# Performance work log

Measured on AMD Instinct MI355X. Metric: run time of the kernel, lower is better.

## Reference

```python
import math
import jax, jax.numpy as jnp
import numpy as np

LAMBDA_TV = 0.005
LAMBDA_WAV = 0.005
MAX_ITER = 15
LEVELS = 3
TV_ITERS = 5  # prox_tv called with num_iter=5 in forward
S2 = math.sqrt(2.0)


def _fft2c(x):
    # x: (B, 2, H, W) real/imag channels -> centered 2D FFT, same layout
    xc = x[:, 0] + 1j * x[:, 1]
    kc = jnp.fft.fftshift(
        jnp.fft.fft2(jnp.fft.ifftshift(xc, axes=(-2, -1)), norm='ortho'),
        axes=(-2, -1))
    return jnp.stack([kc.real, kc.imag], axis=1)


def _ifft2c(x):
    xc = x[:, 0] + 1j * x[:, 1]
    ic = jnp.fft.fftshift(
        jnp.fft.ifft2(jnp.fft.ifftshift(xc, axes=(-2, -1)), norm='ortho'),
        axes=(-2, -1))
    return jnp.stack([ic.real, ic.imag], axis=1)


def _grad(x):
    # x: (N, 1, H, W) -> forward differences, (N, 2, H, W); last row/col zero
    dx = jnp.pad(x[:, :, :, 1:] - x[:, :, :, :-1], ((0, 0), (0, 0), (0, 0), (0, 1)))
    dy = jnp.pad(x[:, :, 1:, :] - x[:, :, :-1, :], ((0, 0), (0, 0), (0, 1), (0, 0)))
    return jnp.concatenate([dx, dy], axis=1)


def _div(p):
    # adjoint of _grad with the exact boundary handling of the torch code
    px, py = p[:, 0:1], p[:, 1:2]
    div_x = jnp.concatenate(
        [px[:, :, :, 0:1], px[:, :, :, 1:-1] - px[:, :, :, :-2], -px[:, :, :, -2:-1]],
        axis=-1)
    div_y = jnp.concatenate(
        [py[:, :, 0:1, :], py[:, :, 1:-1, :] - py[:, :, :-2, :], -py[:, :, -2:-1, :]],
        axis=2)
    return div_x + div_y


def _prox_tv(x, lam):
    # Chambolle dual iteration, applied per channel (vectorized over B*C)
    B, C, H, W = x.shape
    xc = x.reshape(B * C, 1, H, W)
    tau = 0.25

    def body(p, _):
        g = _grad(xc - lam * _div(p))
        pn = p + tau * g
        nrm = jnp.sqrt(jnp.sum(pn * pn, axis=1, keepdims=True) + 1e-8)
        return pn / jnp.maximum(nrm, 1.0), None

    p0 = jnp.zeros((B * C, 2, H, W), x.dtype)
    p, _ = jax.lax.scan(body, p0, None, length=TV_ITERS)
    return (xc - lam * _div(p)).reshape(B, C, H, W)


def _dwt2(x):
    x_lo = (x[:, :, :, ::2] + x[:, :, :, 1::2]) / S2
    x_hi = (x[:, :, :, ::2] - x[:, :, :, 1::2]) / S2
    ll = (x_lo[:, :, ::2] + x_lo[:, :, 1::2]) / S2
    lh = (x_lo[:, :, ::2] - x_lo[:, :, 1::2]) / S2
    hl = (x_hi[:, :, ::2] + x_hi[:, :, 1::2]) / S2
    hh = (x_hi[:, :, ::2] - x_hi[:, :, 1::2]) / S2
    return ll, (lh, hl, hh)


def _interleave(even, odd, axis):
    s = jnp.stack([even, odd], axis=axis + 1)
    shp = list(even.shape)
    shp[axis] *= 2
    return s.reshape(shp)


def _idwt2(ll, lh, hl, hh):
    x_lo = _interleave((ll + lh) / S2, (ll - lh) / S2, axis=2)  # rows
    x_hi = _interleave((hl + hh) / S2, (hl - hh) / S2, axis=2)
    return _interleave((x_lo + x_hi) / S2, (x_lo - x_hi) / S2, axis=3)  # cols


def _soft(x, t):
    return jnp.sign(x) * jnp.maximum(jnp.abs(x) - t, 0.0)


def setup_inputs() -> dict:
    key = jax.random.key(0)
    k1, k2 = jax.random.split(key)
    B, H, W = 16, 320, 320
    y = jax.random.normal(k1, (B, 2, H, W), jnp.float32)
    mask = (jax.random.uniform(k2, (B, 1, H, W)) < 0.3).astype(jnp.float32)
    return {"y": y, "mask": mask}


def reference(y, mask):
    def step(carry, _):
        x, z, t = carry
        # projected gradient for data fidelity (step_size = 1.0)
        g = _ifft2c(mask * (mask * _fft2c(z) - y))
        z_step = z - g
        # TV prox
        x_tv = _prox_tv(z_step, LAMBDA_TV)
        # wavelet decomposition + soft-threshold of detail subbands
        cur = x_tv
        details = []
        for _lvl in range(LEVELS):
            cur, d = _dwt2(cur)
            details.append(tuple(_soft(c, LAMBDA_WAV) for c in d))
        x_new = cur
        for d in reversed(details):
            x_new = _idwt2(x_new, *d)
        # FISTA momentum
        t_new = (1.0 + jnp.sqrt(1.0 + 4.0 * t * t)) / 2.0
        z_new = x_new + (t - 1.0) / t_new * (x_new - x)
        return (x_new, z_new, t_new), None

    x0 = _ifft2c(y)
    (x, _, _), _ = jax.lax.scan(jax.checkpoint(step), (x0, x0, jnp.float32(1.0)),
                                None, length=MAX_ITER)
    return x
```

## Files before the change

kernel.cpp:

```cpp
#include <hip/hip_runtime.h>
#include <math.h>

constexpr int WID  = 320;
constexpr int HWc  = 320 * 320;
constexpr int NIMG = 16;
constexpr int NSL  = 32;
constexpr int NTOT = NIMG * 2 * HWc;
constexpr float LAM_TV  = 0.005f;
constexpr float LAM_WAV = 0.005f;

__device__ __forceinline__ float softt(float v) {
    float a = fmaxf(fabsf(v) - LAM_WAV, 0.f);
    return copysignf(a, v);
}

__device__ __forceinline__ float fast_rsq(float x) {
    float r;
    asm volatile("v_rsq_f32 %0, %1" : "=v"(r) : "v"(x));
    return r;
}

struct Tw { float tc, ts; float stc[6], sts[6]; };

__global__ void build_tw(float* tb) {
    const int lane = threadIdx.x;
#pragma unroll
    for (int g = 0; g < 2; g++) {
        const float sgn = g ? 1.f : -1.f;
        float* p = tb + g * 14 * 64;
        float ts, tc;
        __sincosf(sgn * 6.283185307179586f * (float)lane / 320.f, &ts, &tc);
        p[lane] = tc; p[64 + lane] = ts;
#pragma unroll
        for (int s = 0; s < 6; s++) {
            int h = 32 >> s;
            int j = lane & (h - 1);
            float ang = sgn * 3.14159265358979323f * (float)j / (float)h;
            float ss, cc;
            __sincosf(ang, &ss, &cc);
            p[(2 + s) * 64 + lane] = cc;
            p[(8 + s) * 64 + lane] = ss;
        }
    }
}

__device__ __forceinline__ Tw load_tw(const float* __restrict__ tb, int lane) {
    Tw tw;
    tw.tc = tb[lane];
    tw.ts = tb[64 + lane];
#pragma unroll
    for (int s = 0; s < 6; s++) {
        tw.stc[s] = tb[(2 + s) * 64 + lane];
        tw.sts[s] = tb[(8 + s) * 64 + lane];
    }
    return tw;
}

template<int SGN>
__device__ __forceinline__ void fft320_core(const float (&vr)[5], const float (&vi)[5],
                                            float (&Cr)[5], float (&Ci)[5],
                                            const Tw& tw, int lane) {
    const float cw1 = 0.30901699437494745f, sw1 = 0.9510565162951535f;
    const float cw2 = -0.8090169943749475f, sw2 = 0.5877852522924731f;
    const float cwt[5] = {1.f, cw1, cw2, cw2, cw1};
    const float swt[5] = {0.f, sw1, sw2, -sw2, -sw1};
    Cr[0] = vr[0] + vr[1] + vr[2] + vr[3] + vr[4];
    Ci[0] = vi[0] + vi[1] + vi[2] + vi[3] + vi[4];
#pragma unroll
    for (int k = 1; k < 5; k++) {
        float ar = vr[0], ai = vi[0];
#pragma unroll
        for (int m = 1; m < 5; m++) {
            int j = (m * k) % 5;
            float wr_ = cwt[j], wi_ = (float)SGN * swt[j];
            ar += vr[m] * wr_ - vi[m] * wi_;
            ai += vr[m] * wi_ + vi[m] * wr_;
        }
        Cr[k] = ar; Ci[k] = ai;
    }
    float twr = 1.f, twi = 0.f;
#pragma unroll
    for (int k = 1; k < 5; k++) {
        float nr = twr * tw.tc - twi * tw.ts;
        twi = twr * tw.ts + twi * tw.tc;
        twr = nr;
        float r = Cr[k] * twr - Ci[k] * twi;
        Ci[k]   = Cr[k] * twi + Ci[k] * twr;
        Cr[k]   = r;
    }
#pragma unroll
    for (int s = 0; s < 6; s++) {
        int h = 32 >> s;
        bool up = (lane & h) != 0;
#pragma unroll
        for (int k = 0; k < 5; k++) {
            float orr = __shfl_xor(Cr[k], h);
            float oii = __shfl_xor(Ci[k], h);
            if (up) {
                float dr = orr - Cr[k], di = oii - Ci[k];
                Cr[k] = dr * tw.stc[s] - di * tw.sts[s];
                Ci[k] = dr * tw.sts[s] + di * tw.stc[s];
            } else {
                Cr[k] += orr;
                Ci[k] += oii;
            }
        }
    }
}

template<int SGN, int EPI>
__global__ __launch_bounds__(256) void fft_row(const float* __restrict__ in,
                                               float* __restrict__ out,
                                               const float* __restrict__ aux1,
                                               float* __restrict__ out2,
                                               const float* __restrict__ twb) {
    const int lane = threadIdx.x & 63;
    const int wv   = threadIdx.x >> 6;
    const int L    = blockIdx.x * 4 + wv;
    const int img  = L / 320;
    const int l    = L - img * 320;
    const size_t ibase = (size_t)img * 2 * HWc;
    const float* pre = in + ibase + (size_t)l * WID;
    const float* pim = pre + HWc;
    const int k1 = (int)(__brev((unsigned)lane) >> 26);

    Tw tw = load_tw(twb, lane);

    float vr[5], vi[5];
    const float sgn_in = (lane & 1) ? -1.f : 1.f;
#pragma unroll
    for (int m = 0; m < 5; m++) {
        int n = lane + 64 * m;
        vr[m] = sgn_in * pre[n];
        vi[m] = sgn_in * pim[n];
    }
    float zr[5], zi[5];
    if (EPI == 2) {
#pragma unroll
        for (int k = 0; k < 5; k++) {
            int idxs = 5 * k1 + k + l * WID;
            zr[k] = aux1[ibase + idxs];
            zi[k] = aux1[ibase + HWc + idxs];
        }
    }

    float Cr[5], Ci[5];
    fft320_core<SGN>(vr, vi, Cr, Ci, tw, lane);

    float* qre = out + ibase + (size_t)l * WID;
    float* qim = qre + HWc;
    const float scale = 0.05590169943749474f;
#pragma unroll
    for (int k = 0; k < 5; k++) {
        int kout = 5 * k1 + k;
        float s2 = (kout & 1) ? -scale : scale;
        float re = s2 * Cr[k];
        float im = s2 * Ci[k];
        const int idxs = kout + l * WID;
        if (EPI == 2) {
            re = zr[k] - re;
            im = zi[k] - im;
        }
        qre[kout] = re;
        qim[kout] = im;
        if (EPI == 3) {
            out2[ibase + idxs]       = re;
            out2[ibase + HWc + idxs] = im;
        }
    }
}

constexpr int CB   = 8;
constexpr int CPAD = CB + 1;

template<int SGN>
__device__ __forceinline__ void fft_line_lds(float (*tile)[320][CPAD], int cl,
                                             int lane, const Tw& tw) {
    float vr[5], vi[5], Cr[5], Ci[5];
    const float sgn_in = (lane & 1) ? -1.f : 1.f;
#pragma unroll
    for (int m = 0; m < 5; m++) {
        int n = lane + 64 * m;
        vr[m] = sgn_in * tile[0][n][cl];
        vi[m] = sgn_in * tile[1][n][cl];
    }
    fft320_core<SGN>(vr, vi, Cr, Ci, tw, lane);
    const int k1 = (int)(__brev((unsigned)lane) >> 26);
    const float scale = 0.05590169943749474f;
#pragma unroll
    for (int k = 0; k < 5; k++) {
        int kout = 5 * k1 + k;
        float s2 = (kout & 1) ? -scale : scale;
        tile[0][kout][cl] = s2 * Cr[k];
        tile[1][kout][cl] = s2 * Ci[k];
    }
}

template<int MODE>
__global__ __launch_bounds__(512) void fft_col(const float* __restrict__ in,
                                               float* __restrict__ out,
                                               const float* __restrict__ y,
                                               const float* __restrict__ mask,
                                               const float* __restrict__ twb) {
    __shared__ float tile[2][320][CPAD];
    const int tid = threadIdx.x;
    const int bpi = WID / CB;
    const int img = blockIdx.x / bpi;
    const int c0  = (blockIdx.x - img * bpi) * CB;
    const size_t ibase = (size_t)img * 2 * HWc;
    constexpr int C4 = CB / 4;
    constexpr int NE = 320 * C4;

#pragma unroll
    for (int comp = 0; comp < 2; comp++) {
        const float* p = in + ibase + (size_t)comp * HWc + c0;
        for (int i = tid; i < NE; i += 512) {
            int row = i >> 1, cg = (i & 1) << 2;
            float4 v = *(const float4*)(p + row * WID + cg);
            float* t = &tile[comp][row][cg];
            t[0] = v.x; t[1] = v.y; t[2] = v.z; t[3] = v.w;
        }
    }
    __syncthreads();

    const int lane = tid & 63;
    const int wv   = tid >> 6;

    if (MODE == 1) {
        Tw twf = load_tw(twb, lane);
        fft_line_lds<-1>(tile, wv, lane, twf);
        __syncthreads();
        const float* pm  = mask + (size_t)img * HWc + c0;
        const float* pyr = y + ibase + c0;
        const float* pyi = y + ibase + HWc + c0;
        for (int i = tid; i < NE; i += 512) {
            int row = i >> 1, cg = (i & 1) << 2;
            float4 m4 = *(const float4*)(pm  + row * WID + cg);
            float4 yr = *(const float4*)(pyr + row * WID + cg);
            float4 yi = *(const float4*)(pyi + row * WID + cg);
            float* tr = &tile[0][row][cg];
            float* ti = &tile[1][row][cg];
            tr[0] = m4.x * (m4.x * tr[0] - yr.x);
            tr[1] = m4.y * (m4.y * tr[1] - yr.y);
            tr[2] = m4.z * (m4.z * tr[2] - yr.z);
            tr[3] = m4.w * (m4.w * tr[3] - yr.w);
            ti[0] = m4.x * (m4.x * ti[0] - yi.x);
            ti[1] = m4.y * (m4.y * ti[1] - yi.y);
            ti[2] = m4.z * (m4.z * ti[2] - yi.z);
            ti[3] = m4.w * (m4.w * ti[3] - yi.w);
        }
        __syncthreads();
    }
    {
        Tw twi = load_tw(twb + 14 * 64, lane);
        fft_line_lds<1>(tile, wv, lane, twi);
    }
    __syncthreads();
#pragma unroll
    for (int comp = 0; comp < 2; comp++) {
        float* p = out + ibase + (size_t)comp * HWc + c0;
        for (int i = tid; i < NE; i += 512) {
            int row = i >> 1, cg = (i & 1) << 2;
            const float* t = &tile[comp][row][cg];
            *(float4*)(p + row * WID + cg) = make_float4(t[0], t[1], t[2], t[3]);
        }
    }
}

constexpr int HALO = 4;
constexpr int TIR = 8;
constexpr int TVR = TIR + 2 * HALO;
constexpr int TIC = 48;
constexpr int TCOLS = 7;
constexpr int TROWS = WID / TIR;
constexpr int TPS = TROWS * TCOLS;

template<bool EDGE>
__device__ __forceinline__ void tv_core(const float* __restrict__ g, int gi0, int gj,
                                        float (&uf)[TIR]) {
    float z_[TVR], px_[TVR], py_[TVR];
    const bool colin = !EDGE || ((unsigned)gj < (unsigned)WID);
#pragma unroll
    for (int r = 0; r < TVR; r++) {
        int gi = gi0 + r;
        float v = 0.f;
        if (!EDGE) {
            v = g[gi * WID + gj];
        } else {
            bool in = colin && ((unsigned)gi < (unsigned)WID);
            if (in) v = g[gi * WID + gj];
        }
        z_[r] = v; px_[r] = 0.f; py_[r] = 0.f;
    }
    const bool gj_le0 = EDGE && (gj <= 0);
    const bool gj_hi  = EDGE && (gj >= WID - 1);
    const bool gx_on  = !EDGE || (gj < WID - 1);

#pragma clang loop unroll(disable)
    for (int it = 0; it < 5; it++) {
        float ucur, unext;
        {
            float pxm = __shfl_up(px_[0], 1);
            float divx, divy;
            if (!EDGE) {
                divx = px_[0] - pxm;
                divy = 0.f;
            } else {
                int gi = gi0;
                divx = gj_le0 ? px_[0] : (gj_hi ? -pxm : px_[0] - pxm);
                divy = (gi <= 0) ? py_[0] : ((gi >= WID - 1) ? -py_[0] : 0.f);
            }
            ucur = z_[0] - LAM_TV * (divx + divy);
        }
#pragma unroll
        for (int r = 0; r < TVR - 1; r++) {
            {
                float pxm = __shfl_up(px_[r + 1], 1);
                float divx, divy;
                if (!EDGE) {
                    divx = px_[r + 1] - pxm;
                    divy = py_[r + 1] - py_[r];
                } else {
                    int gi1 = gi0 + r + 1;
                    divx = gj_le0 ? px_[r + 1] : (gj_hi ? -pxm : px_[r + 1] - pxm);
                    divy = (gi1 <= 0) ? py_[r + 1]
                         : ((gi1 >= WID - 1) ? -py_[r] : py_[r + 1] - py_[r]);
                }
                unext = z_[r + 1] - LAM_TV * (divx + divy);
            }
            {
                float un = __shfl_down(ucur, 1);
                float gx, gy;
                if (!EDGE) {
                    gx = un - ucur;
                    gy = unext - ucur;
                } else {
                    int gi = gi0 + r;
                    gx = gx_on ? un - ucur : 0.f;
                    gy = (gi < WID - 1) ? unext - ucur : 0.f;
                }
                float px = fmaf(0.25f, gx, px_[r]);
                float py = fmaf(0.25f, gy, py_[r]);
                float n2 = fmaf(px, px, fmaf(py, py, 1e-8f));
                float inv = fminf(fast_rsq(n2), 1.f);
                px_[r] = px * inv;
                py_[r] = py * inv;
            }
            ucur = unext;
        }
        {
            float un = __shfl_down(ucur, 1);
            float gx = gx_on ? un - ucur : 0.f;
            float px = fmaf(0.25f, gx, px_[TVR - 1]);
            float py = py_[TVR - 1];
            float n2 = fmaf(px, px, fmaf(py, py, 1e-8f));
            float inv = fminf(fast_rsq(n2), 1.f);
            px_[TVR - 1] = px * inv;
            py_[TVR - 1] = py * inv;
        }
    }
#pragma unroll
    for (int r = HALO; r < TVR - HALO; r++) {
        float pxm = __shfl_up(px_[r], 1);
        float divx, divy;
        if (!EDGE) {
            divx = px_[r] - pxm;
            divy = py_[r] - py_[r - 1];
        } else {
            int gi = gi0 + r;
            divx = gj_le0 ? px_[r] : (gj_hi ? -pxm : px_[r] - pxm);
            divy = (gi <= 0) ? py_[r]
                 : ((gi >= WID - 1) ? -py_[r - 1] : py_[r] - py_[r - 1]);
        }
        uf[r - HALO] = z_[r] - LAM_TV * (divx + divy);
    }
}

__global__ __launch_bounds__(256) void tv_wav_fista(const float* __restrict__ zs,
                                                    float* __restrict__ x,
                                                    float* __restrict__ z,
                                                    float beta) {
    const int lane = threadIdx.x & 63;
    const int wv   = __builtin_amdgcn_readfirstlane(threadIdx.x >> 6);
    const int w    = blockIdx.x * 4 + wv;
    const int sl   = w / TPS;
    const int rem  = w - sl * TPS;
    const int trow = rem / TCOLS;
    const int tcol = rem - trow * TCOLS;
    const int gi0  = trow * TIR - HALO;
    const int gj   = tcol * TIC - 8 + lane;
    const float* g = zs + (size_t)sl * HWc;

    float uf[TIR];
    const bool interior = (trow >= 1) && (trow <= TROWS - 2) &&
                          (tcol >= 1) && (tcol <= TCOLS - 2);
    if (interior) tv_core<false>(g, gi0, gj, uf);
    else          tv_core<true >(g, gi0, gj, uf);

    const float sc1 = (lane & 1) ? -1.f : 1.f;
    const float sc2 = (lane & 2) ? -1.f : 1.f;
    const float sc3 = (lane & 4) ? -1.f : 1.f;

    float ll1[4], lh1[4], hl1[4], hh1[4];
#pragma unroll
    for (int k = 0; k < 4; k++) {
        float a0 = uf[2 * k], a1 = uf[2 * k + 1];
        float n0 = __shfl_xor(a0, 1), n1 = __shfl_xor(a1, 1);
        float h0 = a0 + n0, d0 = sc1 * (a0 - n0);
        float h1 = a1 + n1, d1 = sc1 * (a1 - n1);
        ll1[k] = (h0 + h1) * 0.5f;
        lh1[k] = softt((h0 - h1) * 0.5f);
        hl1[k] = softt((d0 + d1) * 0.5f);
        hh1[k] = softt((d0 - d1) * 0.5f);
    }
    float ll2[2], lh2[2], hl2[2], hh2[2];
#pragma unroll
    for (int k = 0; k < 2; k++) {
        float a0 = ll1[2 * k], a1 = ll1[2 * k + 1];
        float n0 = __shfl_xor(a0, 2), n1 = __shfl_xor(a1, 2);
        float h0 = a0 + n0, d0 = sc2 * (a0 - n0);
        float h1 = a1 + n1, d1 = sc2 * (a1 - n1);
        ll2[k] = (h0 + h1) * 0.5f;
        lh2[k] = softt((h0 - h1) * 0.5f);
        hl2[k] = softt((d0 + d1) * 0.5f);
        hh2[k] = softt((d0 - d1) * 0.5f);
    }
    float ll3, lh3, hl3, hh3;
    {
        float a0 = ll2[0], a1 = ll2[1];
        float n0 = __shfl_xor(a0, 4), n1 = __shfl_xor(a1, 4);
        float h0 = a0 + n0, d0 = sc3 * (a0 - n0);
        float h1 = a1 + n1, d1 = sc3 * (a1 - n1);
        ll3 = (h0 + h1) * 0.5f;
        lh3 = softt((h0 - h1) * 0.5f);
        hl3 = softt((d0 + d1) * 0.5f);
        hh3 = softt((d0 - d1) * 0.5f);
    }
    float l2p[2];
    l2p[0] = 0.5f * ((ll3 + lh3) + sc3 * (hl3 + hh3));
    l2p[1] = 0.5f * ((ll3 - lh3) + sc3 * (hl3 - hh3));
    float l1p[4];
#pragma unroll
    for (int k = 0; k < 2; k++) {
        l1p[2 * k]     = 0.5f * ((l2p[k] + lh2[k]) + sc2 * (hl2[k] + hh2[k]));
        l1p[2 * k + 1] = 0.5f * ((l2p[k] - lh2[k]) + sc2 * (hl2[k] - hh2[k]));
    }
    float xn[TIR];
#pragma unroll
    for (int k = 0; k < 4; k++) {
        xn[2 * k]     = 0.5f * ((l1p[k] + lh1[k]) + sc1 * (hl1[k] + hh1[k]));
        xn[2 * k + 1] = 0.5f * ((l1p[k] - lh1[k]) + sc1 * (hl1[k] - hh1[k]));
    }

    const bool wcol = (lane >= 8) && (lane < 56) && ((unsigned)gj < (unsigned)WID);
    float* px = x + (size_t)sl * HWc;
    float* pz = z + (size_t)sl * HWc;
    const int gi_int0 = trow * TIR;
#pragma unroll
    for (int i = 0; i < TIR; i++) {
        int off = (gi_int0 + i) * WID + gj;
        float xo = wcol ? px[off] : 0.f;
        float zn = xn[i] + beta * (xn[i] - xo);
        if (wcol) {
            px[off] = xn[i];
            pz[off] = zn;
        }
    }
}

extern "C" void kernel_launch(void* const* d_in, const int* in_sizes, int n_in,
                              void* d_out, int out_size, void* d_ws, size_t ws_size,
                              hipStream_t stream) {
    const float* y    = (const float*)d_in[0];
    const float* mask = (const float*)d_in[1];
    float* x = (float*)d_out;

    float* ws = (float*)d_ws;
    float* z  = ws;
    float* t1 = ws + (size_t)NTOT;
    float* t2 = ws + 2 * (size_t)NTOT;
    float* tw = ws + 3 * (size_t)NTOT;
    float* twF = tw;
    float* twI = tw + 14 * 64;

    const int ROW_BLKS = (NIMG * 320) / 4;
    const int COL_BLKS = NIMG * (WID / CB);
    const int TV_BLKS  = (NSL * TPS) / 4;

    build_tw<<<1, 64, 0, stream>>>(tw);

    fft_col<0><<<COL_BLKS, 512, 0, stream>>>(y, t1, nullptr, nullptr, twF);
    fft_row<1, 3><<<ROW_BLKS, 256, 0, stream>>>(t1, x, nullptr, z, twI);

    float t = 1.f;
    for (int it = 0; it < 15; it++) {
        fft_row<-1, 0><<<ROW_BLKS, 256, 0, stream>>>(z, t1, nullptr, nullptr, twF);
        fft_col<1><<<COL_BLKS, 512, 0, stream>>>(t1, t2, y, mask, twF);
        fft_row<1, 2><<<ROW_BLKS, 256, 0, stream>>>(t2, t1, z, nullptr, twI);

        float tn   = (1.f + sqrtf(1.f + 4.f * t * t)) * 0.5f;
        float beta = (t - 1.f) / tn;
        t = tn;
        tv_wav_fista<<<TV_BLKS, 256, 0, stream>>>(t1, x, z, beta);
    }
    (void)in_sizes; (void)n_in; (void)out_size; (void)ws_size;
}
```

Baseline: 1.294 ms.

## Batch TV shuffles, group edge tiles contiguously, skip z store on final iteration

The Chambolle TV loop is restructured so each pass computes all row shuffles first, then all u values, then all down-shuffles, instead of a serial row-by-row dependency chain. This exposes more instruction-level parallelism at the cost of more live registers. Wave-to-tile mapping is reordered so edge tiles come first and interior tiles are contiguous, which cuts wave divergence between the EDGE and non-EDGE template paths within a block. The last FISTA iteration uses a variant that skips reading old x and writing z, since z is not used afterwards.

```diff
diff --git a/kernel.cpp b/kernel.cpp
--- a/kernel.cpp
+++ b/kernel.cpp
@@ -274,6 +274,7 @@
 constexpr int TCOLS = 7;
 constexpr int TROWS = WID / TIR;
 constexpr int TPS = TROWS * TCOLS;
+constexpr int NEDGE = 2 * TCOLS + 2 * (TROWS - 2);
 
 template<bool EDGE>
 __device__ __forceinline__ void tv_core(const float* __restrict__ g, int gi0, int gj,
@@ -298,70 +299,52 @@
 
 #pragma clang loop unroll(disable)
     for (int it = 0; it < 5; it++) {
-        float ucur, unext;
-        {
-            float pxm = __shfl_up(px_[0], 1);
+        float u_[TVR], sh[TVR];
+#pragma unroll
+        for (int r = 0; r < TVR; r++) sh[r] = __shfl_up(px_[r], 1);
+#pragma unroll
+        for (int r = 0; r < TVR; r++) {
             float divx, divy;
             if (!EDGE) {
-                divx = px_[0] - pxm;
-                divy = 0.f;
+                divx = px_[r] - sh[r];
+                divy = (r > 0) ? py_[r] - py_[r - 1] : 0.f;
             } else {
-                int gi = gi0;
-                divx = gj_le0 ? px_[0] : (gj_hi ? -pxm : px_[0] - pxm);
-                divy = (gi <= 0) ? py_[0] : ((gi >= WID - 1) ? -py_[0] : 0.f);
+                int gi = gi0 + r;
+                divx = gj_le0 ? px_[r] : (gj_hi ? -sh[r] : px_[r] - sh[r]);
+                float pym = (r > 0) ? py_[r - 1] : py_[0];
+                divy = (gi <= 0) ? py_[r]
+                     : ((gi >= WID - 1) ? -pym : py_[r] - pym);
             }
-            ucur = z_[0] - LAM_TV * (divx + divy);
-        }
-#pragma unroll
-        for (int r = 0; r < TVR - 1; r++) {
-            {
-                float pxm = __shfl_up(px_[r + 1], 1);
-                float divx, divy;
-                if (!EDGE) {
-                    divx = px_[r + 1] - pxm;
-                    divy = py_[r + 1] - py_[r];
-                } else {
-                    int gi1 = gi0 + r + 1;
-                    divx = gj_le0 ? px_[r + 1] : (gj_hi ? -pxm : px_[r + 1] - pxm);
-                    divy = (gi1 <= 0) ? py_[r + 1]
-                         : ((gi1 >= WID - 1) ? -py_[r] : py_[r + 1] - py_[r]);
-                }
-                unext = z_[r + 1] - LAM_TV * (divx + divy);
+            u_[r] = z_[r] - LAM_TV * (divx + divy);
+        }
+#pragma unroll
+        for (int r = 0; r < TVR; r++) sh[r] = __shfl_down(u_[r], 1);
+#pragma unroll
+        for (int r = 0; r < TVR; r++) {
+            float gx, gy;
+            if (!EDGE) {
+                gx = sh[r] - u_[r];
+                gy = (r < TVR - 1) ? u_[r + 1] - u_[r] : 0.f;
+            } else {
+                int gi = gi0 + r;
+                float ub = (r < TVR - 1) ? u_[r + 1] : u_[r];
+                gx = gx_on ? sh[r] - u_[r] : 0.f;
+                gy = (gi < WID - 1 && r < TVR - 1) ? ub - u_[r] : 0.f;
             }
-            {
-                float un = __shfl_down(ucur, 1);
-                float gx, gy;
-                if (!EDGE) {
-                    gx = un - ucur;
-                    gy = unext - ucur;
-                } else {
-                    int gi = gi0 + r;
-                    gx = gx_on ? un - ucur : 0.f;
-                    gy = (gi < WID - 1) ? unext - ucur : 0.f;
-                }
-                float px = fmaf(0.25f, gx, px_[r]);
-                float py = fmaf(0.25f, gy, py_[r]);
-                float n2 = fmaf(px, px, fmaf(py, py, 1e-8f));
-                float inv = fminf(fast_rsq(n2), 1.f);
-                px_[r] = px * inv;
-                py_[r] = py * inv;
-            }
-            ucur = unext;
-        }
-        {
-            float un = __shfl_down(ucur, 1);
-            float gx = gx_on ? un - ucur : 0.f;
-            float px = fmaf(0.25f, gx, px_[TVR - 1]);
-            float py = py_[TVR - 1];
+            float px = fmaf(0.25f, gx, px_[r]);
+            float py = fmaf(0.25f, gy, py_[r]);
             float n2 = fmaf(px, px, fmaf(py, py, 1e-8f));
             float inv = fminf(fast_rsq(n2), 1.f);
-            px_[TVR - 1] = px * inv;
-            py_[TVR - 1] = py * inv;
-        }
-    }
+            px_[r] = px * inv;
+            py_[r] = py * inv;
+        }
+    }
+    float shf[TIR];
+#pragma unroll
+    for (int r = HALO; r < TVR - HALO; r++) shf[r - HALO] = __shfl_up(px_[r], 1);
 #pragma unroll
     for (int r = HALO; r < TVR - HALO; r++) {
-        float pxm = __shfl_up(px_[r], 1);
+        float pxm = shf[r - HALO];
         float divx, divy;
         if (!EDGE) {
             divx = px_[r] - pxm;
@@ -376,6 +359,7 @@
     }
 }
 
+template<bool STOREZ>
 __global__ __launch_bounds__(256) void tv_wav_fista(const float* __restrict__ zs,
                                                     float* __restrict__ x,
                                                     float* __restrict__ z,
@@ -385,17 +369,26 @@
     const int w    = blockIdx.x * 4 + wv;
     const int sl   = w / TPS;
     const int rem  = w - sl * TPS;
-    const int trow = rem / TCOLS;
-    const int tcol = rem - trow * TCOLS;
+    int trow, tcol;
+    if (rem < 2 * TCOLS) {
+        trow = (rem < TCOLS) ? 0 : (TROWS - 1);
+        tcol = (rem < TCOLS) ? rem : rem - TCOLS;
+    } else if (rem < NEDGE) {
+        int e = rem - 2 * TCOLS;
+        trow = 1 + (e % (TROWS - 2));
+        tcol = (e < TROWS - 2) ? 0 : (TCOLS - 1);
+    } else {
+        int i2 = rem - NEDGE;
+        trow = 1 + i2 / (TCOLS - 2);
+        tcol = 1 + i2 % (TCOLS - 2);
+    }
     const int gi0  = trow * TIR - HALO;
     const int gj   = tcol * TIC - 8 + lane;
     const float* g = zs + (size_t)sl * HWc;
 
     float uf[TIR];
-    const bool interior = (trow >= 1) && (trow <= TROWS - 2) &&
-                          (tcol >= 1) && (tcol <= TCOLS - 2);
-    if (interior) tv_core<false>(g, gi0, gj, uf);
-    else          tv_core<true >(g, gi0, gj, uf);
+    if (rem >= NEDGE) tv_core<false>(g, gi0, gj, uf);
+    else              tv_core<true >(g, gi0, gj, uf);
 
     const float sc1 = (lane & 1) ? -1.f : 1.f;
     const float sc2 = (lane & 2) ? -1.f : 1.f;
@@ -459,11 +452,15 @@
 #pragma unroll
     for (int i = 0; i < TIR; i++) {
         int off = (gi_int0 + i) * WID + gj;
-        float xo = wcol ? px[off] : 0.f;
-        float zn = xn[i] + beta * (xn[i] - xo);
-        if (wcol) {
-            px[off] = xn[i];
-            pz[off] = zn;
+        if (STOREZ) {
+            float xo = wcol ? px[off] : 0.f;
+            float zn = xn[i] + beta * (xn[i] - xo);
+            if (wcol) {
+                px[off] = xn[i];
+                pz[off] = zn;
+            }
+        } else {
+            if (wcol) px[off] = xn[i];
         }
     }
 }
@@ -501,7 +498,10 @@
         float tn   = (1.f + sqrtf(1.f + 4.f * t * t)) * 0.5f;
         float beta = (t - 1.f) / tn;
         t = tn;
-        tv_wav_fista<<<TV_BLKS, 256, 0, stream>>>(t1, x, z, beta);
+        if (it < 14)
+            tv_wav_fista<true ><<<TV_BLKS, 256, 0, stream>>>(t1, x, z, beta);
+        else
+            tv_wav_fista<false><<<TV_BLKS, 256, 0, stream>>>(t1, x, z, beta);
     }
     (void)in_sizes; (void)n_in; (void)out_size; (void)ws_size;
 }
```

Result: no change. 1.278 ms (-1.2%).
